# Kernel optimization log

Measured on AMD Instinct MI355X. Metric: run time of the kernel, lower is better.

## Reference

```python
import jax, jax.numpy as jnp
import numpy as np

B, S, D, H = 2, 2048, 1024, 16
DK = D // H
NEG = -1000000000.0


def setup_inputs() -> dict:
    key = jax.random.key(0)
    ks = jax.random.split(key, 12)
    s = 1.0 / np.sqrt(D)
    return {
        "Q": jax.random.normal(ks[0], (B, S, D), jnp.float32),
        "K": jax.random.normal(ks[1], (B, S, D), jnp.float32),
        "V": jax.random.normal(ks[2], (B, S, D), jnp.float32),
        "attn_mask": jnp.zeros((B, S, S), jnp.bool_),
        "WQ_w": jax.random.normal(ks[3], (D, D), jnp.float32) * s,
        "WQ_b": jnp.zeros((D,), jnp.float32),
        "WK_w": jax.random.normal(ks[4], (D, D), jnp.float32) * s,
        "WK_b": jnp.zeros((D,), jnp.float32),
        "WV_w": jax.random.normal(ks[5], (D, D), jnp.float32) * s,
        "WV_b": jnp.zeros((D,), jnp.float32),
        "fc_w": jax.random.normal(ks[6], (D, D), jnp.float32) * s,
        "fc_b": jnp.zeros((D,), jnp.float32),
    }


def reference(Q, K, V, attn_mask, WQ_w, WQ_b, WK_w, WK_b, WV_w, WV_b, fc_w, fc_b):
    b = Q.shape[0]
    # linear projections (torch Linear: x @ W^T + b), split heads -> [b, h, s, dk]
    q = (Q @ WQ_w.T + WQ_b).reshape(b, -1, H, DK).transpose(0, 2, 1, 3)
    k = (K @ WK_w.T + WK_b).reshape(b, -1, H, DK).transpose(0, 2, 1, 3)
    v = (V @ WV_w.T + WV_b).reshape(b, -1, H, DK).transpose(0, 2, 1, 3)
    # scaled dot-product attention with masked_fill
    scores = jnp.einsum("bhqd,bhkd->bhqk", q, k) / jnp.sqrt(jnp.float32(DK))
    scores = jnp.where(attn_mask[:, None, :, :], NEG, scores)
    attn_weights = jax.nn.softmax(scores, axis=-1)  # dropout p=0 -> identity
    attn = jnp.einsum("bhqk,bhkd->bhqd", attn_weights, v)
    attn = attn.transpose(0, 2, 1, 3).reshape(b, -1, H * DK)
    output = attn @ fc_w.T + fc_b
    return output, attn_weights
```

## Files before the change

### kernel.cpp

```cpp
#include <hip/hip_runtime.h>
#include <cstdint>
#include <cstddef>

constexpr int CB = 2;
constexpr int CS = 2048;
constexpr int CD = 1024;
constexpr int CH = 16;
constexpr int CDK = 64;
constexpr float NEGV = -1000000000.0f;
constexpr float QSCALE = 0.18033688011112042f;

typedef __bf16 bf16x8 __attribute__((ext_vector_type(8)));
typedef float f32x4 __attribute__((ext_vector_type(4)));
typedef unsigned short u16x8 __attribute__((ext_vector_type(8)));
typedef unsigned short u16x4 __attribute__((ext_vector_type(4)));

static __device__ __forceinline__ unsigned short f2bf(float x) {
  unsigned int u = __float_as_uint(x);
  u += 0x7fffu + ((u >> 16) & 1u);
  return (unsigned short)(u >> 16);
}
static __device__ __forceinline__ bf16x8 bc8(u16x8 u) {
  return __builtin_bit_cast(bf16x8, u);
}
static __device__ __forceinline__ f32x4 mfma16(bf16x8 a, bf16x8 b, f32x4 c) {
  return __builtin_amdgcn_mfma_f32_16x16x32_bf16(a, b, c, 0, 0, 0);
}

struct CvtArgs {
  const float* src[7];
  unsigned short* dst[7];
  int n4[7];
};

__global__ __launch_bounds__(256) void cvt_all(CvtArgs a) {
  const int r = blockIdx.y;
  const float* __restrict__ in = a.src[r];
  unsigned short* __restrict__ out = a.dst[r];
  const int n4 = a.n4[r];
  const int stride = gridDim.x * 256;
  for (int i = blockIdx.x * 256 + threadIdx.x; i < n4; i += stride) {
    float4 v = reinterpret_cast<const float4*>(in)[i];
    u16x4 o;
    o[0] = f2bf(v.x); o[1] = f2bf(v.y); o[2] = f2bf(v.z); o[3] = f2bf(v.w);
    reinterpret_cast<u16x4*>(out)[i] = o;
  }
}

__global__ __launch_bounds__(256) void mask_scan(const unsigned char* __restrict__ mask,
                                                 unsigned int* __restrict__ tab) {
  __shared__ unsigned int w;
  if (threadIdx.x == 0) w = 0;
  __syncthreads();
  const int b = blockIdx.y, qt = blockIdx.x;
  const int t = threadIdx.x;
  const int row = qt * 64 + (t >> 2);
  const unsigned char* p = mask + ((size_t)b * CS + row) * CS + (t & 3) * 512;
  unsigned int local = 0;
#pragma unroll
  for (int i = 0; i < 8; ++i) {
    const uint4* q = reinterpret_cast<const uint4*>(p + i * 64);
    const uint4 a = q[0], b4 = q[1], c = q[2], d = q[3];
    if ((a.x | a.y | a.z | a.w | b4.x | b4.y | b4.z | b4.w |
         c.x | c.y | c.z | c.w | d.x | d.y | d.z | d.w) != 0)
      local |= 1u << ((t & 3) * 8 + i);
  }
  if (local) atomicOr(&w, local);
  __syncthreads();
  if (t == 0) tab[b * 32 + qt] = w;
}

constexpr int GK = 1024, GNT = GK / 32;

struct QKVArgs {
  const unsigned short* X[3];
  const unsigned short* W[3];
  const float* bias[3];
  unsigned short* out[3];
  float osc[3];
};

template <int BN, typename EPI>
__device__ __forceinline__ void gemm_body(const unsigned short* __restrict__ X,
                                          const unsigned short* __restrict__ Wt,
                                          EPI epi) {
  __shared__ unsigned short lA[2][128 * 32];
  __shared__ unsigned short lB[2][BN * 32];
  const int tid = threadIdx.x, lane = tid & 63, wid = tid >> 6;
  const int fr = lane & 15, fc = lane >> 4;
  const int mbase = blockIdx.y * 128, nbase = blockIdx.x * BN;
  const int wm = (wid & 1) * 64, wn = (wid >> 1) * (BN / 2);

  const int srow = lane >> 2;
  const int sslot = (lane & 3) ^ (srow & 3);
  const int cA = wid * 2;
  const unsigned short* a0 = X + (size_t)(mbase + cA * 16 + srow) * GK + sslot * 8;
  const unsigned short* b0;
  if constexpr (BN == 128) b0 = Wt + (size_t)(nbase + cA * 16 + srow) * GK + sslot * 8;
  else                     b0 = Wt + (size_t)(nbase + wid * 16 + srow) * GK + sslot * 8;

  auto stage = [&](int buf, int k0) {
#pragma unroll
    for (int c = 0; c < 2; ++c)
      __builtin_amdgcn_global_load_lds(
          (const __attribute__((address_space(1))) void*)(a0 + (size_t)c * 16 * GK + k0),
          (__attribute__((address_space(3))) void*)((char*)&lA[buf][0] + (cA + c) * 1024), 16, 0, 0);
    if constexpr (BN == 128) {
#pragma unroll
      for (int c = 0; c < 2; ++c)
        __builtin_amdgcn_global_load_lds(
            (const __attribute__((address_space(1))) void*)(b0 + (size_t)c * 16 * GK + k0),
            (__attribute__((address_space(3))) void*)((char*)&lB[buf][0] + (cA + c) * 1024), 16, 0, 0);
    } else {
      __builtin_amdgcn_global_load_lds(
          (const __attribute__((address_space(1))) void*)(b0 + k0),
          (__attribute__((address_space(3))) void*)((char*)&lB[buf][0] + wid * 1024), 16, 0, 0);
    }
  };

  constexpr int NJ = BN / 32;
  f32x4 acc[4][NJ] = {};
  stage(0, 0);
  __syncthreads();
  for (int t = 0; t < GNT; ++t) {
    if (t + 1 < GNT) stage((t + 1) & 1, (t + 1) * 32);
    const int buf = t & 1;
    bf16x8 af[4], bfv[NJ];
#pragma unroll
    for (int i = 0; i < 4; ++i) {
      const int row = wm + i * 16 + fr;
      af[i] = bc8(*reinterpret_cast<const u16x8*>(&lA[buf][row * 32 + ((fc ^ (row & 3)) * 8)]));
    }
#pragma unroll
    for (int j = 0; j < NJ; ++j) {
      const int row = wn + j * 16 + fr;
      bfv[j] = bc8(*reinterpret_cast<const u16x8*>(&lB[buf][row * 32 + ((fc ^ (row & 3)) * 8)]));
    }
#pragma unroll
    for (int i = 0; i < 4; ++i)
#pragma unroll
      for (int j = 0; j < NJ; ++j)
        acc[i][j] = mfma16(af[i], bfv[j], acc[i][j]);
    __syncthreads();
  }

#pragma unroll
  for (int j = 0; j < NJ; ++j) {
    const int colb = nbase + wn + j * 16 + fr;
#pragma unroll
    for (int i = 0; i < 4; ++i) {
#pragma unroll
      for (int r = 0; r < 4; ++r) {
        const int rowb = mbase + wm + i * 16 + fc * 4 + r;
        epi(rowb, colb, acc[i][j][r]);
      }
    }
  }
}

__global__ __launch_bounds__(256, 3) void gemm_qkv(QKVArgs a) {
  const int z = blockIdx.z;
  const float* bias = a.bias[z];
  unsigned short* out = a.out[z];
  const float osc = a.osc[z];
  gemm_body<128>(a.X[z], a.W[z], [&](int rowb, int colb, float av) {
    const float v = (av + bias[colb]) * osc;
    const int bb = rowb >> 11, sr = rowb & (CS - 1);
    const int hh = colb >> 6, cc = colb & (CDK - 1);
    const size_t bh = (size_t)bb * CH + hh;
    if (z == 0) {
      out[(bh * CS + sr) * CDK + cc] = f2bf(v);
    } else if (z == 1) {
      const int kt = sr >> 6, ww = sr & 63, g = ww >> 4, fr2 = ww & 15;
      const int half = cc >> 5, fc2 = (cc >> 3) & 3, zz = cc & 7;
      out[(bh * 256 + kt * 8 + g * 2 + half) * 512 + (fc2 * 16 + fr2) * 8 + zz] = f2bf(v);
    } else {
      const int kt = sr >> 6, kk = sr & 63;
      const int c = kk >> 5, k32 = kk & 31;
      const int fcv = (k32 >> 2) & 3;
      const int zv = ((k32 >> 4) << 2) | (k32 & 3);
      const int g = cc >> 4, fr2 = cc & 15;
      out[(bh * 256 + kt * 8 + c * 4 + g) * 512 + (fr2 + 16 * fcv) * 8 + zv] = f2bf(v);
    }
  });
}

__global__ __launch_bounds__(256) void gemm_fc(const unsigned short* __restrict__ X,
                                               const unsigned short* __restrict__ Wt,
                                               const float* __restrict__ bias,
                                               float* __restrict__ out) {
  gemm_body<64>(X, Wt, [&](int rowb, int colb, float av) {
    out[(size_t)rowb * CD + colb] = av + bias[colb];
  });
}

__global__ __launch_bounds__(256, 4) void attn_fused(const unsigned short* __restrict__ qh,
                                                     const unsigned short* __restrict__ kT,
                                                     const unsigned short* __restrict__ vT,
                                                     const unsigned char* __restrict__ mask,
                                                     const unsigned int* __restrict__ dirtytab,
                                                     float* __restrict__ attnw,
                                                     unsigned short* __restrict__ attn_pre) {
  const int tid = threadIdx.x, lane = tid & 63, wid = tid >> 6;
  const int bid = blockIdx.x;
  const int swz = (bid & 7) * 128 + (bid >> 3);
  const int qt = swz & 31, hh = (swz >> 5) & 15, b = swz >> 9;
  const int bh = b * CH + hh;
  const int qw = qt * 64 + wid * 16;
  const int fr = lane & 15, fc = lane >> 4;

  const unsigned int dirtybits = dirtytab[b * 32 + qt];

  const unsigned short* qp = qh + ((size_t)bh * CS + qw + fr) * CDK + fc * 8;
  const bf16x8 aq0 = bc8(*reinterpret_cast<const u16x8*>(qp));
  const bf16x8 aq1 = bc8(*reinterpret_cast<const u16x8*>(qp + 32));

  const unsigned short* kbase = kT + (size_t)bh * 131072 + lane * 8;
  const unsigned short* vbase = vT + (size_t)bh * 131072 + lane * 8;

  u16x8 kreg[8];
  auto loadK = [&](int kt) {
    const unsigned short* p = kbase + (size_t)kt * 4096;
#pragma unroll
    for (int f = 0; f < 8; ++f) kreg[f] = *reinterpret_cast<const u16x8*>(p + f * 512);
  };
  auto qk = [&](f32x4 (&sf)[4]) {
    __builtin_amdgcn_s_setprio(1);
#pragma unroll
    for (int g = 0; g < 4; ++g) {
      f32x4 a = {0.f, 0.f, 0.f, 0.f};
      a = mfma16(bc8(kreg[2 * g]), aq0, a);
      a = mfma16(bc8(kreg[2 * g + 1]), aq1, a);
      sf[g] = a;
    }
    __builtin_amdgcn_s_setprio(0);
  };
  const unsigned char* mq = mask + ((size_t)b * CS + qw + fr) * CS + fc * 4;
  auto maskfix = [&](f32x4 (&sf)[4], int kt) {
#pragma unroll
    for (int g = 0; g < 4; ++g) {
      const uchar4 m4 = *reinterpret_cast<const uchar4*>(mq + kt * 64 + g * 16);
      if (m4.x) sf[g][0] = NEGV;
      if (m4.y) sf[g][1] = NEGV;
      if (m4.z) sf[g][2] = NEGV;
      if (m4.w) sf[g][3] = NEGV;
    }
  };

  float lsum = 0.f;
  loadK(0);
  for (int kt = 0; kt < 32; ++kt) {
    f32x4 sf[4];
    qk(sf);
    if (kt + 1 < 32) loadK(kt + 1);
    if ((dirtybits >> kt) & 1u) maskfix(sf, kt);
#pragma unroll
    for (int g = 0; g < 4; ++g)
      lsum += (exp2f(sf[g][0]) + exp2f(sf[g][1])) + (exp2f(sf[g][2]) + exp2f(sf[g][3]));
  }
  lsum += __shfl_xor(lsum, 16);
  lsum += __shfl_xor(lsum, 32);
  const float linv = 1.0f / lsum;

  f32x4 o[4] = {};
  u16x8 vreg[8];
  auto loadV = [&](int kt) {
    const unsigned short* p = vbase + (size_t)kt * 4096;
#pragma unroll
    for (int f = 0; f < 8; ++f) vreg[f] = *reinterpret_cast<const u16x8*>(p + f * 512);
  };

  float* wrow = attnw + ((size_t)bh * CS + qw + fr) * CS + fc * 4;

  loadK(0);
  for (int kt = 0; kt < 32; ++kt) {
    loadV(kt);

    f32x4 sf[4];
    qk(sf);
    if (kt + 1 < 32) loadK(kt + 1);
    if ((dirtybits >> kt) & 1u) maskfix(sf, kt);

#pragma unroll
    for (int g = 0; g < 4; ++g)
#pragma unroll
      for (int r = 0; r < 4; ++r) sf[g][r] = exp2f(sf[g][r]) * linv;

#pragma unroll
    for (int g = 0; g < 4; ++g)
      __builtin_nontemporal_store(sf[g], reinterpret_cast<f32x4*>(wrow + kt * 64 + g * 16));

    bf16x8 pa[2];
#pragma unroll
    for (int c = 0; c < 2; ++c) {
      unsigned int w0, w1, w2, w3;
      asm("v_cvt_pk_bf16_f32 %0, %1, %2" : "=v"(w0) : "v"(sf[2 * c][0]), "v"(sf[2 * c][1]));
      asm("v_cvt_pk_bf16_f32 %0, %1, %2" : "=v"(w1) : "v"(sf[2 * c][2]), "v"(sf[2 * c][3]));
      asm("v_cvt_pk_bf16_f32 %0, %1, %2" : "=v"(w2) : "v"(sf[2 * c + 1][0]), "v"(sf[2 * c + 1][1]));
      asm("v_cvt_pk_bf16_f32 %0, %1, %2" : "=v"(w3) : "v"(sf[2 * c + 1][2]), "v"(sf[2 * c + 1][3]));
      uint4 uw = {w0, w1, w2, w3};
      pa[c] = __builtin_bit_cast(bf16x8, uw);
    }
    __builtin_amdgcn_s_setprio(1);
#pragma unroll
    for (int g = 0; g < 4; ++g) o[g] = mfma16(pa[0], bc8(vreg[g]), o[g]);
#pragma unroll
    for (int g = 0; g < 4; ++g) o[g] = mfma16(pa[1], bc8(vreg[4 + g]), o[g]);
    __builtin_amdgcn_s_setprio(0);
  }

#pragma unroll
  for (int g = 0; g < 4; ++g)
#pragma unroll
    for (int r = 0; r < 4; ++r) {
      const int q = qw + fc * 4 + r;
      attn_pre[(((size_t)b * CS + q) * CH + hh) * CDK + g * 16 + fr] = f2bf(o[g][r]);
    }
}

extern "C" void kernel_launch(void* const* d_in, const int* in_sizes, int n_in,
                              void* d_out, int out_size, void* d_ws, size_t ws_size,
                              hipStream_t stream) {
  (void)in_sizes; (void)n_in; (void)out_size; (void)ws_size;

  const float* Qf = (const float*)d_in[0];
  const float* Kf = (const float*)d_in[1];
  const float* Vf = (const float*)d_in[2];
  const unsigned char* mask = (const unsigned char*)d_in[3];
  const float* WQw = (const float*)d_in[4];
  const float* WQb = (const float*)d_in[5];
  const float* WKw = (const float*)d_in[6];
  const float* WKb = (const float*)d_in[7];
  const float* WVw = (const float*)d_in[8];
  const float* WVb = (const float*)d_in[9];
  const float* fcw = (const float*)d_in[10];
  const float* fcb = (const float*)d_in[11];

  float* out0 = (float*)d_out;
  float* attnw = out0 + (size_t)CB * CS * CD;

  char* w = (char*)d_ws;
  unsigned short* Qb = (unsigned short*)(w);
  unsigned short* Kb = (unsigned short*)(w + 8388608);
  unsigned short* Vb = (unsigned short*)(w + 2 * 8388608);
  unsigned short* Wqb = (unsigned short*)(w + 3 * 8388608);
  unsigned short* Wkb = Wqb + 1048576;
  unsigned short* Wvb = Wkb + 1048576;
  unsigned short* Wfb = Wvb + 1048576;
  unsigned short* qhp = (unsigned short*)(w + 3 * 8388608 + 4 * 2097152);
  unsigned short* kTp = qhp + 4194304;
  unsigned short* vTp = kTp + 4194304;
  unsigned short* apre = Qb;
  unsigned int* dirtytab = (unsigned int*)Kb;

  const int NELEM4 = (CB * CS * CD) / 4;
  const int WELEM4 = (CD * CD) / 4;

  CvtArgs ca;
  ca.src[0] = Qf;  ca.dst[0] = Qb;  ca.n4[0] = NELEM4;
  ca.src[1] = Kf;  ca.dst[1] = Kb;  ca.n4[1] = NELEM4;
  ca.src[2] = Vf;  ca.dst[2] = Vb;  ca.n4[2] = NELEM4;
  ca.src[3] = WQw; ca.dst[3] = Wqb; ca.n4[3] = WELEM4;
  ca.src[4] = WKw; ca.dst[4] = Wkb; ca.n4[4] = WELEM4;
  ca.src[5] = WVw; ca.dst[5] = Wvb; ca.n4[5] = WELEM4;
  ca.src[6] = fcw; ca.dst[6] = Wfb; ca.n4[6] = WELEM4;
  cvt_all<<<dim3(512, 7), 256, 0, stream>>>(ca);

  QKVArgs qa;
  qa.X[0] = Qb;  qa.W[0] = Wqb; qa.bias[0] = WQb; qa.out[0] = qhp; qa.osc[0] = QSCALE;
  qa.X[1] = Kb;  qa.W[1] = Wkb; qa.bias[1] = WKb; qa.out[1] = kTp; qa.osc[1] = 1.0f;
  qa.X[2] = Vb;  qa.W[2] = Wvb; qa.bias[2] = WVb; qa.out[2] = vTp; qa.osc[2] = 1.0f;
  gemm_qkv<<<dim3(CD / 128, (CB * CS) / 128, 3), 256, 0, stream>>>(qa);

  mask_scan<<<dim3(32, CB), 256, 0, stream>>>(mask, dirtytab);

  attn_fused<<<dim3(1024), 256, 0, stream>>>(qhp, kTp, vTp, mask, dirtytab, attnw, apre);

  gemm_fc<<<dim3(CD / 64, (CB * CS) / 128), 256, 0, stream>>>(apre, Wfb, fcb, out0);
}
```

Baseline: 256.1 us.

## Process two query tiles per block, fusing B's sum pass into A's output pass

Each attention block now handles two adjacent 64-row query tiles. The softmax-denominator pass for tile B shares K loads with the output pass for tile A, so three K sweeps replace the four that two blocks needed before. This halves the grid to 512 blocks and lowers the occupancy hint from 4 to 3 so the extra Q fragments and accumulators fit in registers. The s_setprio hints around the MFMAs are removed. The trade is fewer resident waves and less parallelism in exchange for fewer K-tile loads and fewer QK^T recomputations.

```diff
diff --git a/kernel.cpp b/kernel.cpp
--- a/kernel.cpp
+++ b/kernel.cpp
@@ -194,7 +194,7 @@
   });
 }
 
-__global__ __launch_bounds__(256, 4) void attn_fused(const unsigned short* __restrict__ qh,
+__global__ __launch_bounds__(256, 3) void attn_fused(const unsigned short* __restrict__ qh,
                                                      const unsigned short* __restrict__ kT,
                                                      const unsigned short* __restrict__ vT,
                                                      const unsigned char* __restrict__ mask,
@@ -203,17 +203,23 @@
                                                      unsigned short* __restrict__ attn_pre) {
   const int tid = threadIdx.x, lane = tid & 63, wid = tid >> 6;
   const int bid = blockIdx.x;
-  const int swz = (bid & 7) * 128 + (bid >> 3);
-  const int qt = swz & 31, hh = (swz >> 5) & 15, b = swz >> 9;
+  const int swz = (bid & 7) * 64 + (bid >> 3);
+  const int pairi = swz & 15, hh = (swz >> 4) & 15, b = swz >> 8;
   const int bh = b * CH + hh;
-  const int qw = qt * 64 + wid * 16;
+  const int qtA = pairi * 2, qtB = qtA + 1;
+  const int qwA = qtA * 64 + wid * 16;
+  const int qwB = qwA + 64;
   const int fr = lane & 15, fc = lane >> 4;
 
-  const unsigned int dirtybits = dirtytab[b * 32 + qt];
-
-  const unsigned short* qp = qh + ((size_t)bh * CS + qw + fr) * CDK + fc * 8;
-  const bf16x8 aq0 = bc8(*reinterpret_cast<const u16x8*>(qp));
-  const bf16x8 aq1 = bc8(*reinterpret_cast<const u16x8*>(qp + 32));
+  const unsigned int dirtyA = dirtytab[b * 32 + qtA];
+  const unsigned int dirtyB = dirtytab[b * 32 + qtB];
+
+  const unsigned short* qpA = qh + ((size_t)bh * CS + qwA + fr) * CDK + fc * 8;
+  const bf16x8 aqA0 = bc8(*reinterpret_cast<const u16x8*>(qpA));
+  const bf16x8 aqA1 = bc8(*reinterpret_cast<const u16x8*>(qpA + 32));
+  const unsigned short* qpB = qpA + (size_t)64 * CDK;
+  const bf16x8 aqB0 = bc8(*reinterpret_cast<const u16x8*>(qpB));
+  const bf16x8 aqB1 = bc8(*reinterpret_cast<const u16x8*>(qpB + 32));
 
   const unsigned short* kbase = kT + (size_t)bh * 131072 + lane * 8;
   const unsigned short* vbase = vT + (size_t)bh * 131072 + lane * 8;
@@ -224,19 +230,24 @@
 #pragma unroll
     for (int f = 0; f < 8; ++f) kreg[f] = *reinterpret_cast<const u16x8*>(p + f * 512);
   };
-  auto qk = [&](f32x4 (&sf)[4]) {
-    __builtin_amdgcn_s_setprio(1);
+  u16x8 vreg[8];
+  auto loadV = [&](int kt) {
+    const unsigned short* p = vbase + (size_t)kt * 4096;
+#pragma unroll
+    for (int f = 0; f < 8; ++f) vreg[f] = *reinterpret_cast<const u16x8*>(p + f * 512);
+  };
+  auto qk = [&](const bf16x8 b0, const bf16x8 b1, f32x4 (&sf)[4]) {
 #pragma unroll
     for (int g = 0; g < 4; ++g) {
       f32x4 a = {0.f, 0.f, 0.f, 0.f};
-      a = mfma16(bc8(kreg[2 * g]), aq0, a);
-      a = mfma16(bc8(kreg[2 * g + 1]), aq1, a);
+      a = mfma16(bc8(kreg[2 * g]), b0, a);
+      a = mfma16(bc8(kreg[2 * g + 1]), b1, a);
       sf[g] = a;
     }
-    __builtin_amdgcn_s_setprio(0);
-  };
-  const unsigned char* mq = mask + ((size_t)b * CS + qw + fr) * CS + fc * 4;
-  auto maskfix = [&](f32x4 (&sf)[4], int kt) {
+  };
+  const unsigned char* mqA = mask + ((size_t)b * CS + qwA + fr) * CS + fc * 4;
+  const unsigned char* mqB = mqA + (size_t)64 * CS;
+  auto maskfix = [&](f32x4 (&sf)[4], int kt, const unsigned char* mq) {
 #pragma unroll
     for (int g = 0; g < 4; ++g) {
       const uchar4 m4 = *reinterpret_cast<const uchar4*>(mq + kt * 64 + g * 16);
@@ -246,50 +257,28 @@
       if (m4.w) sf[g][3] = NEGV;
     }
   };
-
-  float lsum = 0.f;
-  loadK(0);
-  for (int kt = 0; kt < 32; ++kt) {
-    f32x4 sf[4];
-    qk(sf);
-    if (kt + 1 < 32) loadK(kt + 1);
-    if ((dirtybits >> kt) & 1u) maskfix(sf, kt);
+  auto esum = [&](const f32x4 (&sf)[4]) {
+    float s = 0.f;
 #pragma unroll
     for (int g = 0; g < 4; ++g)
-      lsum += (exp2f(sf[g][0]) + exp2f(sf[g][1])) + (exp2f(sf[g][2]) + exp2f(sf[g][3]));
-  }
-  lsum += __shfl_xor(lsum, 16);
-  lsum += __shfl_xor(lsum, 32);
-  const float linv = 1.0f / lsum;
-
-  f32x4 o[4] = {};
-  u16x8 vreg[8];
-  auto loadV = [&](int kt) {
-    const unsigned short* p = vbase + (size_t)kt * 4096;
-#pragma unroll
-    for (int f = 0; f < 8; ++f) vreg[f] = *reinterpret_cast<const u16x8*>(p + f * 512);
-  };
-
-  float* wrow = attnw + ((size_t)bh * CS + qw + fr) * CS + fc * 4;
-
-  loadK(0);
-  for (int kt = 0; kt < 32; ++kt) {
-    loadV(kt);
-
-    f32x4 sf[4];
-    qk(sf);
-    if (kt + 1 < 32) loadK(kt + 1);
-    if ((dirtybits >> kt) & 1u) maskfix(sf, kt);
-
+      s += (exp2f(sf[g][0]) + exp2f(sf[g][1])) + (exp2f(sf[g][2]) + exp2f(sf[g][3]));
+    return s;
+  };
+  auto reduce = [&](float s) {
+    s += __shfl_xor(s, 16);
+    s += __shfl_xor(s, 32);
+    return 1.0f / s;
+  };
+  float* wrowA = attnw + ((size_t)bh * CS + qwA + fr) * CS + fc * 4;
+  float* wrowB = wrowA + (size_t)64 * CS;
+  auto p2tail = [&](f32x4 (&sf)[4], const float linv, float* wrow, f32x4 (&o)[4], int kt) {
 #pragma unroll
     for (int g = 0; g < 4; ++g)
 #pragma unroll
       for (int r = 0; r < 4; ++r) sf[g][r] = exp2f(sf[g][r]) * linv;
-
 #pragma unroll
     for (int g = 0; g < 4; ++g)
       __builtin_nontemporal_store(sf[g], reinterpret_cast<f32x4*>(wrow + kt * 64 + g * 16));
-
     bf16x8 pa[2];
 #pragma unroll
     for (int c = 0; c < 2; ++c) {
@@ -301,21 +290,60 @@
       uint4 uw = {w0, w1, w2, w3};
       pa[c] = __builtin_bit_cast(bf16x8, uw);
     }
-    __builtin_amdgcn_s_setprio(1);
 #pragma unroll
     for (int g = 0; g < 4; ++g) o[g] = mfma16(pa[0], bc8(vreg[g]), o[g]);
 #pragma unroll
     for (int g = 0; g < 4; ++g) o[g] = mfma16(pa[1], bc8(vreg[4 + g]), o[g]);
-    __builtin_amdgcn_s_setprio(0);
-  }
-
-#pragma unroll
-  for (int g = 0; g < 4; ++g)
-#pragma unroll
-    for (int r = 0; r < 4; ++r) {
-      const int q = qw + fc * 4 + r;
-      attn_pre[(((size_t)b * CS + q) * CH + hh) * CDK + g * 16 + fr] = f2bf(o[g][r]);
-    }
+  };
+  auto epilogue = [&](const f32x4 (&o)[4], int qw) {
+#pragma unroll
+    for (int g = 0; g < 4; ++g)
+#pragma unroll
+      for (int r = 0; r < 4; ++r) {
+        const int q = qw + fc * 4 + r;
+        attn_pre[(((size_t)b * CS + q) * CH + hh) * CDK + g * 16 + fr] = f2bf(o[g][r]);
+      }
+  };
+
+  float lsA = 0.f;
+  loadK(0);
+  for (int kt = 0; kt < 32; ++kt) {
+    f32x4 sf[4];
+    qk(aqA0, aqA1, sf);
+    if (kt + 1 < 32) loadK(kt + 1);
+    if ((dirtyA >> kt) & 1u) maskfix(sf, kt, mqA);
+    lsA += esum(sf);
+  }
+  const float linvA = reduce(lsA);
+
+  float lsB = 0.f;
+  f32x4 oA[4] = {};
+  loadK(0);
+  for (int kt = 0; kt < 32; ++kt) {
+    loadV(kt);
+    f32x4 sfA[4], sfB[4];
+    qk(aqA0, aqA1, sfA);
+    qk(aqB0, aqB1, sfB);
+    if (kt + 1 < 32) loadK(kt + 1);
+    if ((dirtyA >> kt) & 1u) maskfix(sfA, kt, mqA);
+    if ((dirtyB >> kt) & 1u) maskfix(sfB, kt, mqB);
+    p2tail(sfA, linvA, wrowA, oA, kt);
+    lsB += esum(sfB);
+  }
+  const float linvB = reduce(lsB);
+  epilogue(oA, qwA);
+
+  f32x4 oB[4] = {};
+  loadK(0);
+  for (int kt = 0; kt < 32; ++kt) {
+    loadV(kt);
+    f32x4 sf[4];
+    qk(aqB0, aqB1, sf);
+    if (kt + 1 < 32) loadK(kt + 1);
+    if ((dirtyB >> kt) & 1u) maskfix(sf, kt, mqB);
+    p2tail(sf, linvB, wrowB, oB, kt);
+  }
+  epilogue(oB, qwB);
 }
 
 extern "C" void kernel_launch(void* const* d_in, const int* in_sizes, int n_in,
@@ -374,7 +402,7 @@
 
   mask_scan<<<dim3(32, CB), 256, 0, stream>>>(mask, dirtytab);
 
-  attn_fused<<<dim3(1024), 256, 0, stream>>>(qhp, kTp, vTp, mask, dirtytab, attnw, apre);
+  attn_fused<<<dim3(512), 256, 0, stream>>>(qhp, kTp, vTp, mask, dirtytab, attnw, apre);
 
   gemm_fc<<<dim3(CD / 64, (CB * CS) / 128), 256, 0, stream>>>(apre, Wfb, fcb, out0);
 }
```

New measurement: 261.4 us. +2.0%, slower.
